# Kernel tuning notes

Measured on AMD Instinct MI355X. Metric: run time of the kernel, lower is better.

The kernel has to match this reference:

```python
import jax, jax.numpy as jnp
import numpy as np

EMB = 768
HEADS = 12
HEAD_DIM = EMB // HEADS
SCALE = HEAD_DIM ** -0.5


def setup_inputs() -> dict:
    key = jax.random.key(0)
    kq, kk, kv, kw = jax.random.split(key, 4)
    B, H, N, D = 2, HEADS, 2048, HEAD_DIM
    queries = jax.random.normal(kq, (B, H, N, D), dtype=jnp.float32)
    keys = jax.random.normal(kk, (B, H, N, D), dtype=jnp.float32)
    values = jax.random.normal(kv, (B, H, N, D), dtype=jnp.float32)
    proj_w = jax.random.normal(kw, (EMB, EMB), dtype=jnp.float32) * (EMB ** -0.5)
    proj_b = jnp.zeros((EMB,), dtype=jnp.float32)
    return {"queries": queries, "keys": keys, "values": values,
            "proj_w": proj_w, "proj_b": proj_b}


def reference(queries, keys, values, proj_w, proj_b):
    # energy: [b, h, n, n] -- full quadratic score matrix, as in the original
    energy = jnp.einsum('bhij,bhkj->bhik', queries, keys) * SCALE
    att = jax.nn.softmax(energy, axis=-1)  # att_drop_p=0.0 -> identity
    out = jnp.einsum('bhij,bhjk->bhik', att, values)  # [b, h, n, d]
    b, h, n, d = out.shape
    out = jnp.transpose(out, (0, 2, 1, 3)).reshape(b, n, h * d)  # 'b h n d -> b n (h d)'
    # nn.Linear: x @ W^T + b (projection dropout is inference identity)
    return out @ proj_w.T + proj_b
```

## Files before the change

kernel.cpp:

```cpp
#include <hip/hip_runtime.h>
#include <cstdint>

typedef short bf16x8 __attribute__((ext_vector_type(8)));
typedef float f32x4 __attribute__((ext_vector_type(4)));
typedef uint16_t u16x4 __attribute__((ext_vector_type(4)));

#define MFMA_16x16x32(a, b, c) __builtin_amdgcn_mfma_f32_16x16x32_bf16((a), (b), (c), 0, 0, 0)

static constexpr int BATCH = 2;
static constexpr int HEADS = 12;
static constexpr int NCTX  = 2048;
static constexpr int DH    = 64;
static constexpr int EMB   = 768;

static constexpr float QSCALE = 0.125f * 1.44269504088896340736f;

__device__ __forceinline__ uint16_t f2bf(float x) {
    uint32_t u = __float_as_uint(x);
    u += 0x7FFFu + ((u >> 16) & 1u);
    return (uint16_t)(u >> 16);
}
__device__ __forceinline__ uint32_t cvt_pk_bf16(float lo, float hi) {
    uint32_t r;
    asm("v_cvt_pk_bf16_f32 %0, %1, %2" : "=v"(r) : "v"(lo), "v"(hi));
    return r;
}

__global__ void k_cvtqk(const float* __restrict__ q, const float* __restrict__ k,
                        uint16_t* __restrict__ qb, uint16_t* __restrict__ kb, int n4) {
    int i = blockIdx.x * blockDim.x + threadIdx.x;
    if (i >= n4) return;
    const bool isK = blockIdx.y != 0;
    const float* src = isK ? k : q;
    uint16_t* dst = isK ? kb : qb;
    const float scale = isK ? 1.0f : QSCALE;
    float4 v = reinterpret_cast<const float4*>(src)[i];
    u16x4 hv = {f2bf(v.x * scale), f2bf(v.y * scale), f2bf(v.z * scale), f2bf(v.w * scale)};
    reinterpret_cast<u16x4*>(dst)[i] = hv;
}

__global__ void k_cvt(const float* __restrict__ src, uint16_t* __restrict__ dst, int n4) {
    int i = blockIdx.x * blockDim.x + threadIdx.x;
    if (i >= n4) return;
    float4 v = reinterpret_cast<const float4*>(src)[i];
    u16x4 hv = {f2bf(v.x), f2bf(v.y), f2bf(v.z), f2bf(v.w)};
    reinterpret_cast<u16x4*>(dst)[i] = hv;
}

__global__ __launch_bounds__(256) void k_vt(const float* __restrict__ v,
                                            uint16_t* __restrict__ vt) {
    const int bh = blockIdx.y;
    const int n0 = blockIdx.x * 64;
    const int t  = threadIdx.x;
    __shared__ uint16_t tileT[64][72];

    const int r  = t >> 2;
    const int cc = (t & 3) * 16;
    const float* vp = v + ((size_t)bh * NCTX + n0 + r) * DH + cc;
#pragma unroll
    for (int u = 0; u < 4; ++u) {
        float4 x = reinterpret_cast<const float4*>(vp)[u];
        tileT[cc + 4 * u + 0][r] = f2bf(x.x);
        tileT[cc + 4 * u + 1][r] = f2bf(x.y);
        tileT[cc + 4 * u + 2][r] = f2bf(x.z);
        tileT[cc + 4 * u + 3][r] = f2bf(x.w);
    }
    __syncthreads();
    const int d  = t >> 2;
    const int nc = (t & 3) * 16;
    uint16_t* op = vt + ((size_t)bh * DH + d) * NCTX + n0 + nc;
#pragma unroll
    for (int u = 0; u < 2; ++u) {
        bf16x8 x = *reinterpret_cast<const bf16x8*>(&tileT[d][nc + 8 * u]);
        *reinterpret_cast<bf16x8*>(op + 8 * u) = x;
    }
}

__global__ __launch_bounds__(256) void k_attn(
        const uint16_t* __restrict__ qb, const uint16_t* __restrict__ kb,
        const uint16_t* __restrict__ vt, uint16_t* __restrict__ xb) {
    const int bh = blockIdx.y;
    const int b  = bh / HEADS;
    const int h  = bh % HEADS;
    const int tid = threadIdx.x;
    const int w = tid >> 6;
    const int l = tid & 63;
    const int g = l >> 4;
    const int c = l & 15;

    __shared__ uint16_t Kh_s[64][72];
    __shared__ uint16_t Vt_s[64][72];
    __shared__ uint16_t P_s [4][16][72];

    const int q0 = blockIdx.x * 64 + w * 16;

    const size_t qoff = ((size_t)bh * NCTX + q0 + c) * DH + 8 * g;
    bf16x8 qa[2];
    qa[0] = *reinterpret_cast<const bf16x8*>(qb + qoff);
    qa[1] = *reinterpret_cast<const bf16x8*>(qb + qoff + 32);

    f32x4 zero = {0.f, 0.f, 0.f, 0.f};
    f32x4 o[4] = {zero, zero, zero, zero};
    float m = -1e30f;
    float lsum = 0.f;

    const int srow = tid >> 3;
    const int sch  = tid & 7;

    const uint16_t* kb_b = kb + (size_t)bh * NCTX * DH + srow * DH + sch * 8;
    const uint16_t* vt_b = vt + (size_t)bh * DH * NCTX + srow * NCTX + sch * 8;

    {
        bf16x8 a0 = *reinterpret_cast<const bf16x8*>(kb_b);
        bf16x8 a1 = *reinterpret_cast<const bf16x8*>(kb_b + 32 * DH);
        bf16x8 v0 = *reinterpret_cast<const bf16x8*>(vt_b);
        bf16x8 v1 = *reinterpret_cast<const bf16x8*>(vt_b + 32 * NCTX);
        *reinterpret_cast<bf16x8*>(&Kh_s[srow][sch * 8])      = a0;
        *reinterpret_cast<bf16x8*>(&Kh_s[srow + 32][sch * 8]) = a1;
        *reinterpret_cast<bf16x8*>(&Vt_s[srow][sch * 8])      = v0;
        *reinterpret_cast<bf16x8*>(&Vt_s[srow + 32][sch * 8]) = v1;
    }
    __syncthreads();

    for (int t = 0; t < NCTX / 64; ++t) {
        bf16x8 nk0, nk1, nv0, nv1;
        const bool pf = (t + 1) < NCTX / 64;
        if (pf) {
            const size_t ko = (size_t)(t + 1) * 64 * DH;
            const size_t vo = (size_t)(t + 1) * 64;
            nk0 = *reinterpret_cast<const bf16x8*>(kb_b + ko);
            nk1 = *reinterpret_cast<const bf16x8*>(kb_b + ko + 32 * DH);
            nv0 = *reinterpret_cast<const bf16x8*>(vt_b + vo);
            nv1 = *reinterpret_cast<const bf16x8*>(vt_b + vo + 32 * NCTX);
        }

        f32x4 s[4] = {zero, zero, zero, zero};
        __builtin_amdgcn_s_setprio(1);
#pragma unroll
        for (int nf = 0; nf < 4; ++nf) {
#pragma unroll
            for (int kf = 0; kf < 2; ++kf) {
                bf16x8 bhf = *reinterpret_cast<const bf16x8*>(&Kh_s[nf * 16 + c][kf * 32 + 8 * g]);
                s[nf] = MFMA_16x16x32(bhf, qa[kf], s[nf]);
            }
        }
        __builtin_amdgcn_s_setprio(0);

        float smax = s[0][0];
#pragma unroll
        for (int nf = 0; nf < 4; ++nf)
#pragma unroll
            for (int r = 0; r < 4; ++r) smax = fmaxf(smax, s[nf][r]);
        smax = fmaxf(smax, __shfl_xor(smax, 16));
        smax = fmaxf(smax, __shfl_xor(smax, 32));

        if (!__all(smax <= m + 11.0f)) {
            float mnew = fmaxf(m, smax);
            float corr = __builtin_amdgcn_exp2f(m - mnew);
            m = mnew;
            lsum *= corr;
#pragma unroll
            for (int r = 0; r < 4; ++r) {
                float cr = __shfl(corr, 4 * g + r);
#pragma unroll
                for (int f = 0; f < 4; ++f) o[f][r] *= cr;
            }
        }

#pragma unroll
        for (int nf = 0; nf < 4; ++nf) {
            float p0 = __builtin_amdgcn_exp2f(s[nf][0] - m);
            float p1 = __builtin_amdgcn_exp2f(s[nf][1] - m);
            float p2 = __builtin_amdgcn_exp2f(s[nf][2] - m);
            float p3 = __builtin_amdgcn_exp2f(s[nf][3] - m);
            lsum += (p0 + p1) + (p2 + p3);
            uint2 pk;
            pk.x = cvt_pk_bf16(p0, p1);
            pk.y = cvt_pk_bf16(p2, p3);
            *reinterpret_cast<uint2*>(&P_s[w][c][16 * nf + 4 * g]) = pk;
        }

        bf16x8 pa0 = *reinterpret_cast<const bf16x8*>(&P_s[w][c][8 * g]);
        bf16x8 pa1 = *reinterpret_cast<const bf16x8*>(&P_s[w][c][32 + 8 * g]);
        __builtin_amdgcn_s_setprio(1);
#pragma unroll
        for (int f = 0; f < 4; ++f) {
            bf16x8 b0 = *reinterpret_cast<const bf16x8*>(&Vt_s[f * 16 + c][8 * g]);
            bf16x8 b1 = *reinterpret_cast<const bf16x8*>(&Vt_s[f * 16 + c][32 + 8 * g]);
            o[f] = MFMA_16x16x32(pa0, b0, o[f]);
            o[f] = MFMA_16x16x32(pa1, b1, o[f]);
        }
        __builtin_amdgcn_s_setprio(0);

        __syncthreads();
        if (pf) {
            *reinterpret_cast<bf16x8*>(&Kh_s[srow][sch * 8])      = nk0;
            *reinterpret_cast<bf16x8*>(&Kh_s[srow + 32][sch * 8]) = nk1;
            *reinterpret_cast<bf16x8*>(&Vt_s[srow][sch * 8])      = nv0;
            *reinterpret_cast<bf16x8*>(&Vt_s[srow + 32][sch * 8]) = nv1;
        }
        __syncthreads();
    }

    lsum += __shfl_xor(lsum, 16);
    lsum += __shfl_xor(lsum, 32);
    const float linv = 1.0f / lsum;

    const size_t xbase = ((size_t)b * NCTX + q0) * EMB + h * DH;
#pragma unroll
    for (int r = 0; r < 4; ++r) {
        float lr = __shfl(linv, 4 * g + r);
#pragma unroll
        for (int f = 0; f < 4; ++f) {
            float v = o[f][r] * lr;
            size_t addr = xbase + (size_t)(4 * g + r) * EMB + f * 16 + c;
            xb[addr] = f2bf(v);
        }
    }
}

__global__ __launch_bounds__(256) void k_proj(
        const uint16_t* __restrict__ xb, const uint16_t* __restrict__ wb,
        const float* __restrict__ bias, float* __restrict__ out) {
    const int tid = threadIdx.x;
    const int w = tid >> 6;
    const int l = tid & 63;
    const int g = l >> 4;
    const int c = l & 15;
    const int m0 = blockIdx.x * 64 + w * 16;
    const int n0 = blockIdx.y * 64;

    __shared__ uint16_t Wh_s[64][40];

    f32x4 zero = {0.f, 0.f, 0.f, 0.f};
    f32x4 acc[4] = {zero, zero, zero, zero};

    const int srow = tid >> 2;
    const int sch  = tid & 3;
    constexpr int KSTEPS = EMB / 32;

    const uint16_t* whp = wb + (size_t)(n0 + srow) * EMB + sch * 8;
    const uint16_t* xhp = xb + (size_t)(m0 + c) * EMB + 8 * g;

    bf16x8 wldh = *reinterpret_cast<const bf16x8*>(whp);
    bf16x8 ah   = *reinterpret_cast<const bf16x8*>(xhp);

    for (int ks = 0; ks < KSTEPS; ++ks) {
        __syncthreads();
        *reinterpret_cast<bf16x8*>(&Wh_s[srow][sch * 8]) = wldh;
        __syncthreads();

        const int ksn = (ks + 1 < KSTEPS) ? (ks + 1) : (KSTEPS - 1);
        bf16x8 wldh_n = *reinterpret_cast<const bf16x8*>(whp + (size_t)ksn * 32);
        bf16x8 ah_n   = *reinterpret_cast<const bf16x8*>(xhp + (size_t)ksn * 32);

        __builtin_amdgcn_s_setprio(1);
#pragma unroll
        for (int nf = 0; nf < 4; ++nf) {
            bf16x8 bhf = *reinterpret_cast<const bf16x8*>(&Wh_s[nf * 16 + c][8 * g]);
            acc[nf] = MFMA_16x16x32(ah, bhf, acc[nf]);
        }
        __builtin_amdgcn_s_setprio(0);

        wldh = wldh_n; ah = ah_n;
    }

#pragma unroll
    for (int nf = 0; nf < 4; ++nf) {
#pragma unroll
        for (int r = 0; r < 4; ++r) {
            int row = m0 + g * 4 + r;
            int col = n0 + nf * 16 + c;
            out[(size_t)row * EMB + col] = acc[nf][r] + bias[col];
        }
    }
}

extern "C" void kernel_launch(void* const* d_in, const int* in_sizes, int n_in,
                              void* d_out, int out_size, void* d_ws, size_t ws_size,
                              hipStream_t stream) {
    const float* q    = (const float*)d_in[0];
    const float* k    = (const float*)d_in[1];
    const float* v    = (const float*)d_in[2];
    const float* pw   = (const float*)d_in[3];
    const float* pb   = (const float*)d_in[4];
    float* out = (float*)d_out;

    const size_t nqkv = (size_t)BATCH * HEADS * NCTX * DH;
    const size_t nx   = (size_t)BATCH * NCTX * EMB;
    const size_t nw   = (size_t)EMB * EMB;

    uint8_t* ws = (uint8_t*)d_ws;
    uint16_t* qb = (uint16_t*)ws;              ws += nqkv * 2;
    uint16_t* kb = (uint16_t*)ws;              ws += nqkv * 2;
    uint16_t* vt = (uint16_t*)ws;              ws += nqkv * 2;
    uint16_t* xb = (uint16_t*)ws;              ws += nx * 2;
    uint16_t* wb = (uint16_t*)ws;              ws += nw * 2;

    k_cvtqk<<<dim3((int)(nqkv / 4 / 256), 2), 256, 0, stream>>>(
        q, k, qb, kb, (int)(nqkv / 4));
    k_cvt<<<(int)(nw / 4 / 256), 256, 0, stream>>>(pw, wb, (int)(nw / 4));
    k_vt<<<dim3(NCTX / 64, BATCH * HEADS), 256, 0, stream>>>(v, vt);

    k_attn<<<dim3(NCTX / 64, BATCH * HEADS), 256, 0, stream>>>(qb, kb, vt, xb);

    k_proj<<<dim3((BATCH * NCTX) / 64, EMB / 64), 256, 0, stream>>>(xb, wb, pb, out);
}
```

Before: 84.33 us.

## Fuse Q bf16 conversion into attention and double-buffer K/V shared tiles

Q is now read as fp32 and scaled/converted to bf16 inside the attention kernel, removing the separate Q conversion pass and its intermediate buffer traffic. K and V shared-memory tiles are double-buffered so the next tile can be written without a barrier before the store, dropping one __syncthreads per iteration. The doubled LDS footprint may reduce the number of resident blocks per CU.

```diff
diff --git a/kernel.cpp b/kernel.cpp
--- a/kernel.cpp
+++ b/kernel.cpp
@@ -24,19 +24,6 @@
     uint32_t r;
     asm("v_cvt_pk_bf16_f32 %0, %1, %2" : "=v"(r) : "v"(lo), "v"(hi));
     return r;
-}
-
-__global__ void k_cvtqk(const float* __restrict__ q, const float* __restrict__ k,
-                        uint16_t* __restrict__ qb, uint16_t* __restrict__ kb, int n4) {
-    int i = blockIdx.x * blockDim.x + threadIdx.x;
-    if (i >= n4) return;
-    const bool isK = blockIdx.y != 0;
-    const float* src = isK ? k : q;
-    uint16_t* dst = isK ? kb : qb;
-    const float scale = isK ? 1.0f : QSCALE;
-    float4 v = reinterpret_cast<const float4*>(src)[i];
-    u16x4 hv = {f2bf(v.x * scale), f2bf(v.y * scale), f2bf(v.z * scale), f2bf(v.w * scale)};
-    reinterpret_cast<u16x4*>(dst)[i] = hv;
 }
 
 __global__ void k_cvt(const float* __restrict__ src, uint16_t* __restrict__ dst, int n4) {
@@ -77,7 +64,7 @@
 }
 
 __global__ __launch_bounds__(256) void k_attn(
-        const uint16_t* __restrict__ qb, const uint16_t* __restrict__ kb,
+        const float* __restrict__ q, const uint16_t* __restrict__ kb,
         const uint16_t* __restrict__ vt, uint16_t* __restrict__ xb) {
     const int bh = blockIdx.y;
     const int b  = bh / HEADS;
@@ -88,16 +75,27 @@
     const int g = l >> 4;
     const int c = l & 15;
 
-    __shared__ uint16_t Kh_s[64][72];
-    __shared__ uint16_t Vt_s[64][72];
-    __shared__ uint16_t P_s [4][16][72];
+    __shared__ uint16_t K_s[2][64][72];
+    __shared__ uint16_t V_s[2][64][72];
+    __shared__ uint16_t P_s[4][16][72];
 
     const int q0 = blockIdx.x * 64 + w * 16;
 
-    const size_t qoff = ((size_t)bh * NCTX + q0 + c) * DH + 8 * g;
     bf16x8 qa[2];
-    qa[0] = *reinterpret_cast<const bf16x8*>(qb + qoff);
-    qa[1] = *reinterpret_cast<const bf16x8*>(qb + qoff + 32);
+    {
+        const float* qp = q + ((size_t)bh * NCTX + q0 + c) * DH + 8 * g;
+#pragma unroll
+        for (int kf = 0; kf < 2; ++kf) {
+            float4 x0 = *reinterpret_cast<const float4*>(qp + kf * 32);
+            float4 x1 = *reinterpret_cast<const float4*>(qp + kf * 32 + 4);
+            bf16x8 f;
+            f[0] = (short)f2bf(x0.x * QSCALE); f[1] = (short)f2bf(x0.y * QSCALE);
+            f[2] = (short)f2bf(x0.z * QSCALE); f[3] = (short)f2bf(x0.w * QSCALE);
+            f[4] = (short)f2bf(x1.x * QSCALE); f[5] = (short)f2bf(x1.y * QSCALE);
+            f[6] = (short)f2bf(x1.z * QSCALE); f[7] = (short)f2bf(x1.w * QSCALE);
+            qa[kf] = f;
+        }
+    }
 
     f32x4 zero = {0.f, 0.f, 0.f, 0.f};
     f32x4 o[4] = {zero, zero, zero, zero};
@@ -115,14 +113,17 @@
         bf16x8 a1 = *reinterpret_cast<const bf16x8*>(kb_b + 32 * DH);
         bf16x8 v0 = *reinterpret_cast<const bf16x8*>(vt_b);
         bf16x8 v1 = *reinterpret_cast<const bf16x8*>(vt_b + 32 * NCTX);
-        *reinterpret_cast<bf16x8*>(&Kh_s[srow][sch * 8])      = a0;
-        *reinterpret_cast<bf16x8*>(&Kh_s[srow + 32][sch * 8]) = a1;
-        *reinterpret_cast<bf16x8*>(&Vt_s[srow][sch * 8])      = v0;
-        *reinterpret_cast<bf16x8*>(&Vt_s[srow + 32][sch * 8]) = v1;
+        *reinterpret_cast<bf16x8*>(&K_s[0][srow][sch * 8])      = a0;
+        *reinterpret_cast<bf16x8*>(&K_s[0][srow + 32][sch * 8]) = a1;
+        *reinterpret_cast<bf16x8*>(&V_s[0][srow][sch * 8])      = v0;
+        *reinterpret_cast<bf16x8*>(&V_s[0][srow + 32][sch * 8]) = v1;
     }
     __syncthreads();
 
     for (int t = 0; t < NCTX / 64; ++t) {
+        const int cur = t & 1;
+        const int nxt = cur ^ 1;
+
         bf16x8 nk0, nk1, nv0, nv1;
         const bool pf = (t + 1) < NCTX / 64;
         if (pf) {
@@ -140,7 +141,7 @@
         for (int nf = 0; nf < 4; ++nf) {
 #pragma unroll
             for (int kf = 0; kf < 2; ++kf) {
-                bf16x8 bhf = *reinterpret_cast<const bf16x8*>(&Kh_s[nf * 16 + c][kf * 32 + 8 * g]);
+                bf16x8 bhf = *reinterpret_cast<const bf16x8*>(&K_s[cur][nf * 16 + c][kf * 32 + 8 * g]);
                 s[nf] = MFMA_16x16x32(bhf, qa[kf], s[nf]);
             }
         }
@@ -185,19 +186,18 @@
         __builtin_amdgcn_s_setprio(1);
 #pragma unroll
         for (int f = 0; f < 4; ++f) {
-            bf16x8 b0 = *reinterpret_cast<const bf16x8*>(&Vt_s[f * 16 + c][8 * g]);
-            bf16x8 b1 = *reinterpret_cast<const bf16x8*>(&Vt_s[f * 16 + c][32 + 8 * g]);
+            bf16x8 b0 = *reinterpret_cast<const bf16x8*>(&V_s[cur][f * 16 + c][8 * g]);
+            bf16x8 b1 = *reinterpret_cast<const bf16x8*>(&V_s[cur][f * 16 + c][32 + 8 * g]);
             o[f] = MFMA_16x16x32(pa0, b0, o[f]);
             o[f] = MFMA_16x16x32(pa1, b1, o[f]);
         }
         __builtin_amdgcn_s_setprio(0);
 
-        __syncthreads();
         if (pf) {
-            *reinterpret_cast<bf16x8*>(&Kh_s[srow][sch * 8])      = nk0;
-            *reinterpret_cast<bf16x8*>(&Kh_s[srow + 32][sch * 8]) = nk1;
-            *reinterpret_cast<bf16x8*>(&Vt_s[srow][sch * 8])      = nv0;
-            *reinterpret_cast<bf16x8*>(&Vt_s[srow + 32][sch * 8]) = nv1;
+            *reinterpret_cast<bf16x8*>(&K_s[nxt][srow][sch * 8])      = nk0;
+            *reinterpret_cast<bf16x8*>(&K_s[nxt][srow + 32][sch * 8]) = nk1;
+            *reinterpret_cast<bf16x8*>(&V_s[nxt][srow][sch * 8])      = nv0;
+            *reinterpret_cast<bf16x8*>(&V_s[nxt][srow + 32][sch * 8]) = nv1;
         }
         __syncthreads();
     }
@@ -291,18 +291,16 @@
     const size_t nw   = (size_t)EMB * EMB;
 
     uint8_t* ws = (uint8_t*)d_ws;
-    uint16_t* qb = (uint16_t*)ws;              ws += nqkv * 2;
     uint16_t* kb = (uint16_t*)ws;              ws += nqkv * 2;
     uint16_t* vt = (uint16_t*)ws;              ws += nqkv * 2;
     uint16_t* xb = (uint16_t*)ws;              ws += nx * 2;
     uint16_t* wb = (uint16_t*)ws;              ws += nw * 2;
 
-    k_cvtqk<<<dim3((int)(nqkv / 4 / 256), 2), 256, 0, stream>>>(
-        q, k, qb, kb, (int)(nqkv / 4));
-    k_cvt<<<(int)(nw / 4 / 256), 256, 0, stream>>>(pw, wb, (int)(nw / 4));
+    k_cvt<<<(int)(nqkv / 4 / 256), 256, 0, stream>>>(k, kb, (int)(nqkv / 4));
+    k_cvt<<<(int)(nw / 4 / 256),   256, 0, stream>>>(pw, wb, (int)(nw / 4));
     k_vt<<<dim3(NCTX / 64, BATCH * HEADS), 256, 0, stream>>>(v, vt);
 
-    k_attn<<<dim3(NCTX / 64, BATCH * HEADS), 256, 0, stream>>>(qb, kb, vt, xb);
+    k_attn<<<dim3(NCTX / 64, BATCH * HEADS), 256, 0, stream>>>(q, kb, vt, xb);
 
     k_proj<<<dim3((BATCH * NCTX) / 64, EMB / 64), 256, 0, stream>>>(xb, wb, pb, out);
 }
```

New measurement: 83.66 us. Within noise of the previous version (-0.8%).
